# Optimization experiments

Hardware: AMD Instinct MI355X
Metric: run time of the kernel (lower is better)

The kernel has to match this reference:

```python
import jax, jax.numpy as jnp
import numpy as np

HIDDEN = 1024

def setup_inputs() -> dict:
    key = jax.random.key(0)
    k1, k2, k3 = jax.random.split(key, 3)
    X = jax.random.normal(k1, (4, 2048, HIDDEN), dtype=jnp.float32)
    W = jax.random.normal(k2, (HIDDEN, 3 * HIDDEN), dtype=jnp.float32) * (1.0 / np.sqrt(HIDDEN))
    b = jax.random.normal(k3, (3 * HIDDEN,), dtype=jnp.float32) * 0.02
    return {"X": X, "W": W, "b": b}

def reference(X, W, b):
    D = X.shape[-1]
    # fused QKV projection: [B,S,3D]
    QKV = jnp.einsum('bsd,de->bse', X, W) + b
    Q, K, V = jnp.split(QKV, 3, axis=-1)
    # full attention scores [B,S,S]
    scores = jnp.einsum('bqd,bkd->bqk', Q, K) / jnp.sqrt(jnp.float32(D))
    attn = jax.nn.softmax(scores, axis=-1)
    out = jnp.einsum('bqk,bkd->bqd', attn, V)
    return out
```

## Files before the change

### kernel.cpp

```cpp
#include <hip/hip_runtime.h>

typedef unsigned short u16;
typedef unsigned int   u32;
typedef __attribute__((ext_vector_type(8)))  short bf16x8;
typedef __attribute__((ext_vector_type(16))) float f32x16;
typedef __attribute__((ext_vector_type(4)))  unsigned short us4;

__device__ __forceinline__ u16 f2bf(float f) {
    union { float f; u32 u; } v; v.f = f;
    u32 u = v.u;
    return (u16)((u + 0x7fffu + ((u >> 16) & 1u)) >> 16);
}
__device__ __forceinline__ float bf2f_lo(u32 p) {
    union { u32 u; float f; } t; t.u = p << 16; return t.f;
}
__device__ __forceinline__ float bf2f_hi(u32 p) {
    union { u32 u; float f; } t; t.u = p & 0xffff0000u; return t.f;
}

__device__ __forceinline__ void gload_lds16(const void* g, void* l) {
    __builtin_amdgcn_global_load_lds((const __attribute__((address_space(1))) u32*)g,
                                     (__attribute__((address_space(3))) u32*)l,
                                     16, 0, 0);
}

template<int MINW, bool OUT_BF16, bool ADD_BIAS, bool PROJ, int MODE>
__global__ __launch_bounds__(256, MINW)
void gemm256(const u16* __restrict__ A, int lda, size_t strA,
             const u16* __restrict__ B, int ldb, size_t strB,
             void* __restrict__ Cv, int ldc, size_t strC,
             u16* __restrict__ Vtp,
             const float* __restrict__ bias, int K, float alpha)
{
    __shared__ __align__(16) u16 As[2][256 * 32];
    __shared__ __align__(16) u16 Bs[2][128 * 32];

    const int tid  = threadIdx.x;
    const int w    = tid >> 6;
    const int lane = tid & 63;
    const int wm   = w >> 1, wn = w & 1;
    const int l31  = lane & 31, lh = lane >> 5;

    const u32 id = blockIdx.x, x = id & 7, j = id >> 3;
    int mb, nb, bb;
    if (MODE == 0) { bb = 0;             mb = 8 * (int)(j & 3) + (int)x;        nb = (int)(j >> 2); }
    else           { bb = (int)(x >> 1); mb = 2 * (int)(j & 3) + (int)(x & 1);  nb = (int)(j >> 2); }
    const int m0 = mb * 256, n0 = nb * 128;

    A += (size_t)bb * strA;
    B += (size_t)bb * strB;

    size_t goffA[4], goffB[2];
#pragma unroll
    for (int h = 0; h < 4; ++h) {
        const int c = h * 256 + w * 64 + lane;
        const int r = c >> 2;
        const int q = ((c & 3) - (r >> 1)) & 3;
        goffA[h] = (size_t)(m0 + r) * lda + q * 8;
    }
#pragma unroll
    for (int h = 0; h < 2; ++h) {
        const int c = h * 256 + w * 64 + lane;
        const int r = c >> 2;
        const int q = ((c & 3) - (r >> 1)) & 3;
        goffB[h] = (size_t)(n0 + r) * ldb + q * 8;
    }

    int offA[4][2], offB[2][2];
#pragma unroll
    for (int i = 0; i < 4; ++i) {
        const int ra = wm * 128 + i * 32 + l31;
#pragma unroll
        for (int ks = 0; ks < 2; ++ks)
            offA[i][ks] = (ra * 4 + ((ks * 2 + lh + (ra >> 1)) & 3)) * 16;
    }
#pragma unroll
    for (int jj = 0; jj < 2; ++jj) {
        const int rb = wn * 64 + jj * 32 + l31;
#pragma unroll
        for (int ks = 0; ks < 2; ++ks)
            offB[jj][ks] = (rb * 4 + ((ks * 2 + lh + (rb >> 1)) & 3)) * 16;
    }

    f32x16 acc[4][2] = {};

#pragma unroll
    for (int h = 0; h < 4; ++h)
        gload_lds16(A + goffA[h], (char*)As[0] + (h * 256 + w * 64) * 16);
#pragma unroll
    for (int h = 0; h < 2; ++h)
        gload_lds16(B + goffB[h], (char*)Bs[0] + (h * 256 + w * 64) * 16);

    int cur = 0;
    for (int k0 = 0; k0 < K; k0 += 32) {
        __syncthreads();

        const int nk = k0 + 32;
        if (nk < K) {
#pragma unroll
            for (int h = 0; h < 4; ++h)
                gload_lds16(A + goffA[h] + nk, (char*)As[cur ^ 1] + (h * 256 + w * 64) * 16);
#pragma unroll
            for (int h = 0; h < 2; ++h)
                gload_lds16(B + goffB[h] + nk, (char*)Bs[cur ^ 1] + (h * 256 + w * 64) * 16);
        }

        const u16* Ac = As[cur]; const u16* Bc = Bs[cur];
#pragma unroll
        for (int ks = 0; ks < 2; ++ks) {
            bf16x8 af[4], bfr[2];
#pragma unroll
            for (int i = 0; i < 4; ++i)
                af[i] = *(const bf16x8*)((const char*)Ac + offA[i][ks]);
#pragma unroll
            for (int jj = 0; jj < 2; ++jj)
                bfr[jj] = *(const bf16x8*)((const char*)Bc + offB[jj][ks]);
#pragma unroll
            for (int i = 0; i < 4; ++i)
#pragma unroll
                for (int jj = 0; jj < 2; ++jj)
                    acc[i][jj] = __builtin_amdgcn_mfma_f32_32x32x16_bf16(
                        af[i], bfr[jj], acc[i][jj], 0, 0, 0);
        }
        cur ^= 1;
    }

    float bval[2];
    if (ADD_BIAS) {
#pragma unroll
        for (int jj = 0; jj < 2; ++jj) bval[jj] = bias[n0 + wn * 64 + jj * 32 + l31];
    }
    const bool vt = PROJ && (n0 >= 2048);
#pragma unroll
    for (int i = 0; i < 4; ++i) {
        const int rowb = m0 + wm * 128 + i * 32 + 4 * lh;
#pragma unroll
        for (int jj = 0; jj < 2; ++jj) {
            const int col = n0 + wn * 64 + jj * 32 + l31;
            if (vt) {
                const int b = rowb >> 11;
                u16* dst = Vtp + ((size_t)(b * 1024) + (col - 2048)) * 2048 + (rowb & 2047);
#pragma unroll
                for (int g = 0; g < 4; ++g) {
                    us4 o = { f2bf(acc[i][jj][4 * g + 0] + bval[jj]),
                              f2bf(acc[i][jj][4 * g + 1] + bval[jj]),
                              f2bf(acc[i][jj][4 * g + 2] + bval[jj]),
                              f2bf(acc[i][jj][4 * g + 3] + bval[jj]) };
                    *(us4*)(dst + 8 * g) = o;
                }
            } else {
#pragma unroll
                for (int r = 0; r < 16; ++r) {
                    const int row = rowb + (r & 3) + 8 * (r >> 2);
                    float v = acc[i][jj][r] * alpha;
                    if (ADD_BIAS) v += bval[jj];
                    if (OUT_BF16)
                        ((u16*)Cv)[(size_t)bb * strC + (size_t)row * ldc + col] = f2bf(v);
                    else
                        ((float*)Cv)[(size_t)bb * strC + (size_t)row * ldc + col] = v;
                }
            }
        }
    }
}

__global__ __launch_bounds__(512, 4)
void gemm128s(const u16* __restrict__ A, int lda, size_t strA,
              const u16* __restrict__ B, int ldb, size_t strB,
              float* __restrict__ C, int ldc, size_t strC)
{
    __shared__ __align__(16) char smem[65536];

    const int tid  = threadIdx.x;
    const int sub  = tid >> 8;
    const int t    = tid & 255;
    const int w    = t >> 6;
    const int lane = t & 63;
    const int wm   = w >> 1, wn = w & 1;
    const int l31  = lane & 31, lh = lane >> 5;

    const u32 id = blockIdx.x, x = id & 7, j = id >> 3;
    const int bb = (int)(x >> 1);
    const int mb = 2 * (int)(j & 7) + (int)(x & 1);
    const int nb = (int)(j >> 3);
    const int m0 = mb * 128, n0 = nb * 128;

    A += (size_t)bb * strA + sub * 1024;
    B += (size_t)bb * strB + sub * 1024;

    u16* As = (u16*)(smem + sub * 16384);
    u16* Bs = (u16*)(smem + sub * 16384 + 8192);

    size_t goffA[2], goffB[2];
#pragma unroll
    for (int h = 0; h < 2; ++h) {
        const int c = h * 256 + t;
        const int r = c >> 2;
        const int q = ((c & 3) - (r >> 1)) & 3;
        goffA[h] = (size_t)(m0 + r) * lda + q * 8;
        goffB[h] = (size_t)(n0 + r) * ldb + q * 8;
    }

    int offA[2][2], offB[2][2];
#pragma unroll
    for (int i = 0; i < 2; ++i) {
        const int ra = wm * 64 + i * 32 + l31;
        const int rb = wn * 64 + i * 32 + l31;
#pragma unroll
        for (int ks = 0; ks < 2; ++ks) {
            const int qq = ks * 2 + lh;
            offA[i][ks] = (ra * 4 + ((qq + (ra >> 1)) & 3)) * 16;
            offB[i][ks] = (rb * 4 + ((qq + (rb >> 1)) & 3)) * 16;
        }
    }

    f32x16 acc[2][2] = {};

    for (int k0 = 0; k0 < 1024; k0 += 32) {
#pragma unroll
        for (int h = 0; h < 2; ++h) {
            gload_lds16(A + goffA[h] + k0, (char*)As + (h * 256 + w * 64) * 16);
            gload_lds16(B + goffB[h] + k0, (char*)Bs + (h * 256 + w * 64) * 16);
        }
        __syncthreads();

#pragma unroll
        for (int ks = 0; ks < 2; ++ks) {
            bf16x8 af[2], bfr[2];
#pragma unroll
            for (int i = 0; i < 2; ++i) {
                af[i]  = *(const bf16x8*)((const char*)As + offA[i][ks]);
                bfr[i] = *(const bf16x8*)((const char*)Bs + offB[i][ks]);
            }
#pragma unroll
            for (int i = 0; i < 2; ++i)
#pragma unroll
                for (int jj = 0; jj < 2; ++jj)
                    acc[i][jj] = __builtin_amdgcn_mfma_f32_32x32x16_bf16(
                        af[i], bfr[jj], acc[i][jj], 0, 0, 0);
        }
        __syncthreads();
    }

    float* red = (float*)smem;
    if (sub == 1) {
#pragma unroll
        for (int c = 0; c < 16; ++c) {
            const int i = c >> 3, jj = (c >> 2) & 1, r0 = (c & 3) * 4;
            float4 v = { acc[i][jj][r0 + 0], acc[i][jj][r0 + 1],
                         acc[i][jj][r0 + 2], acc[i][jj][r0 + 3] };
            *(float4*)(red + t * 64 + ((c + t) & 15) * 4) = v;
        }
    }
    __syncthreads();
    if (sub == 0) {
#pragma unroll
        for (int c = 0; c < 16; ++c) {
            const int i = c >> 3, jj = (c >> 2) & 1, r0 = (c & 3) * 4;
            float4 v = *(const float4*)(red + t * 64 + ((c + t) & 15) * 4);
            acc[i][jj][r0 + 0] += v.x; acc[i][jj][r0 + 1] += v.y;
            acc[i][jj][r0 + 2] += v.z; acc[i][jj][r0 + 3] += v.w;
        }
#pragma unroll
        for (int i = 0; i < 2; ++i) {
            const int rowb = m0 + wm * 64 + i * 32 + 4 * lh;
#pragma unroll
            for (int jj = 0; jj < 2; ++jj) {
                const int col = n0 + wn * 64 + jj * 32 + l31;
#pragma unroll
                for (int r = 0; r < 16; ++r) {
                    const int row = rowb + (r & 3) + 8 * (r >> 2);
                    C[(size_t)bb * strC + (size_t)row * ldc + col] = acc[i][jj][r];
                }
            }
        }
    }
}

__global__ __launch_bounds__(256)
void convert_x(const float* __restrict__ X, u16* __restrict__ Xb, int n4)
{
    int i = blockIdx.x * blockDim.x + threadIdx.x;
    if (i < n4) {
        float4 v = ((const float4*)X)[i];
        us4 o = { f2bf(v.x), f2bf(v.y), f2bf(v.z), f2bf(v.w) };
        ((us4*)Xb)[i] = o;
    }
}

__global__ __launch_bounds__(256)
void transpose_w(const float* __restrict__ W, u16* __restrict__ Wt)
{
    __shared__ u16 t[64][65];
    const int k0 = blockIdx.x * 64, n0 = blockIdx.y * 64;
    const int tx = threadIdx.x, ty = threadIdx.y;
#pragma unroll
    for (int i = 0; i < 64; i += 4)
        t[ty + i][tx] = f2bf(W[(size_t)(k0 + ty + i) * 3072 + n0 + tx]);
    __syncthreads();
#pragma unroll
    for (int i = 0; i < 64; i += 4)
        Wt[(size_t)(n0 + ty + i) * 1024 + k0 + tx] = t[tx][ty + i];
}

__global__ __launch_bounds__(256)
void softmax_rows(u16* __restrict__ S)
{
    __shared__ float redm[4], reds[4];
    u16* sr = S + (size_t)blockIdx.x * 2048;
    const int t = threadIdx.x;

    uint4 raw = ((const uint4*)sr)[t];
    float xx[8];
    xx[0] = bf2f_lo(raw.x); xx[1] = bf2f_hi(raw.x);
    xx[2] = bf2f_lo(raw.y); xx[3] = bf2f_hi(raw.y);
    xx[4] = bf2f_lo(raw.z); xx[5] = bf2f_hi(raw.z);
    xx[6] = bf2f_lo(raw.w); xx[7] = bf2f_hi(raw.w);

    float mx = fmaxf(fmaxf(fmaxf(xx[0], xx[1]), fmaxf(xx[2], xx[3])),
                     fmaxf(fmaxf(xx[4], xx[5]), fmaxf(xx[6], xx[7])));
#pragma unroll
    for (int o = 32; o; o >>= 1) mx = fmaxf(mx, __shfl_xor(mx, o));
    if ((t & 63) == 0) redm[t >> 6] = mx;
    __syncthreads();
    mx = fmaxf(fmaxf(redm[0], redm[1]), fmaxf(redm[2], redm[3]));

    float e[8], s = 0.f;
#pragma unroll
    for (int k = 0; k < 8; ++k) { e[k] = __expf(xx[k] - mx); s += e[k]; }
#pragma unroll
    for (int o = 32; o; o >>= 1) s += __shfl_xor(s, o);
    if ((t & 63) == 0) reds[t >> 6] = s;
    __syncthreads();
    s = reds[0] + reds[1] + reds[2] + reds[3];
    const float inv = 1.0f / s;

    uint4 o4;
    o4.x = (u32)f2bf(e[0] * inv) | ((u32)f2bf(e[1] * inv) << 16);
    o4.y = (u32)f2bf(e[2] * inv) | ((u32)f2bf(e[3] * inv) << 16);
    o4.z = (u32)f2bf(e[4] * inv) | ((u32)f2bf(e[5] * inv) << 16);
    o4.w = (u32)f2bf(e[6] * inv) | ((u32)f2bf(e[7] * inv) << 16);
    ((uint4*)sr)[t] = o4;
}

extern "C" void kernel_launch(void* const* d_in, const int* in_sizes, int n_in,
                              void* d_out, int out_size, void* d_ws, size_t ws_size,
                              hipStream_t stream)
{
    const float* X    = (const float*)d_in[0];
    const float* W    = (const float*)d_in[1];
    const float* bias = (const float*)d_in[2];
    float* out = (float*)d_out;
    char* ws = (char*)d_ws;

    u16* QK = (u16*)ws;
    u16* Vt = (u16*)(ws + 33554432);
    u16* S  = (u16*)(ws + 50331648);
    u16* Xb = (u16*)(ws + 50331648);
    u16* Wt = (u16*)(ws + 67108864);

    convert_x<<<8192, 256, 0, stream>>>(X, Xb, 8192 * 1024 / 4);
    transpose_w<<<dim3(16, 48), dim3(64, 4), 0, stream>>>(W, Wt);

    gemm256<3, true, true, true, 0><<<768, 256, 0, stream>>>(
        Xb, 1024, 0, Wt, 1024, 0, QK, 2048, 0, Vt, bias, 1024, 1.0f);

    gemm256<2, true, false, false, 2><<<512, 256, 0, stream>>>(
        QK,        2048, (size_t)2048 * 2048,
        QK + 1024, 2048, (size_t)2048 * 2048,
        S,         2048, (size_t)2048 * 2048,
        nullptr, nullptr, 1024, 0.03125f);

    softmax_rows<<<8192, 256, 0, stream>>>(S);

    gemm128s<<<512, 512, 0, stream>>>(
        S,  2048, (size_t)2048 * 2048,
        Vt, 2048, (size_t)1024 * 2048,
        out, 1024, (size_t)2048 * 1024);
}
```

Baseline: 255.3 us.

## Run score GEMM on split-K 128x128 kernel and merge prep launches

The QK^T score GEMM moves from the 256x128-tile kernel to the 512-thread split-K 128x128 kernel. That kernel is generalized with a K parameter, an alpha scale and an optional bf16 output, and runs with 1024 blocks for more parallelism and occupancy. The X conversion and W transpose kernels are merged into one launch with a block-index branch, and the projection GEMM is specialized with fixed constants. The trade-off is an extra LDS reduction between the two K halves in the score GEMM and smaller tiles with less reuse.

```diff
diff --git a/kernel.cpp b/kernel.cpp
--- a/kernel.cpp
+++ b/kernel.cpp
@@ -24,16 +24,14 @@
                                      16, 0, 0);
 }
 
-template<int MINW, bool OUT_BF16, bool ADD_BIAS, bool PROJ, int MODE>
-__global__ __launch_bounds__(256, MINW)
-void gemm256(const u16* __restrict__ A, int lda, size_t strA,
-             const u16* __restrict__ B, int ldb, size_t strB,
-             void* __restrict__ Cv, int ldc, size_t strC,
-             u16* __restrict__ Vtp,
-             const float* __restrict__ bias, int K, float alpha)
+__global__ __launch_bounds__(256, 3)
+void gemm_proj(const u16* __restrict__ A, const u16* __restrict__ B,
+               u16* __restrict__ QK, u16* __restrict__ Vtp,
+               const float* __restrict__ bias)
 {
     __shared__ __align__(16) u16 As[2][256 * 32];
     __shared__ __align__(16) u16 Bs[2][128 * 32];
+    const int K = 1024, lda = 1024, ldb = 1024;
 
     const int tid  = threadIdx.x;
     const int w    = tid >> 6;
@@ -42,13 +40,9 @@
     const int l31  = lane & 31, lh = lane >> 5;
 
     const u32 id = blockIdx.x, x = id & 7, j = id >> 3;
-    int mb, nb, bb;
-    if (MODE == 0) { bb = 0;             mb = 8 * (int)(j & 3) + (int)x;        nb = (int)(j >> 2); }
-    else           { bb = (int)(x >> 1); mb = 2 * (int)(j & 3) + (int)(x & 1);  nb = (int)(j >> 2); }
+    const int mb = 8 * (int)(j & 3) + (int)x;
+    const int nb = (int)(j >> 2);
     const int m0 = mb * 256, n0 = nb * 128;
-
-    A += (size_t)bb * strA;
-    B += (size_t)bb * strB;
 
     size_t goffA[4], goffB[2];
 #pragma unroll
@@ -126,11 +120,9 @@
     }
 
     float bval[2];
-    if (ADD_BIAS) {
-#pragma unroll
-        for (int jj = 0; jj < 2; ++jj) bval[jj] = bias[n0 + wn * 64 + jj * 32 + l31];
-    }
-    const bool vt = PROJ && (n0 >= 2048);
+#pragma unroll
+    for (int jj = 0; jj < 2; ++jj) bval[jj] = bias[n0 + wn * 64 + jj * 32 + l31];
+    const bool vt = (n0 >= 2048);
 #pragma unroll
     for (int i = 0; i < 4; ++i) {
         const int rowb = m0 + wm * 128 + i * 32 + 4 * lh;
@@ -152,22 +144,19 @@
 #pragma unroll
                 for (int r = 0; r < 16; ++r) {
                     const int row = rowb + (r & 3) + 8 * (r >> 2);
-                    float v = acc[i][jj][r] * alpha;
-                    if (ADD_BIAS) v += bval[jj];
-                    if (OUT_BF16)
-                        ((u16*)Cv)[(size_t)bb * strC + (size_t)row * ldc + col] = f2bf(v);
-                    else
-                        ((float*)Cv)[(size_t)bb * strC + (size_t)row * ldc + col] = v;
+                    QK[(size_t)row * 2048 + col] = f2bf(acc[i][jj][r] + bval[jj]);
                 }
             }
         }
     }
 }
 
+template<bool OUT_BF16>
 __global__ __launch_bounds__(512, 4)
 void gemm128s(const u16* __restrict__ A, int lda, size_t strA,
               const u16* __restrict__ B, int ldb, size_t strB,
-              float* __restrict__ C, int ldc, size_t strC)
+              void* __restrict__ Cv, int ldc, size_t strC,
+              int K, float alpha)
 {
     __shared__ __align__(16) char smem[65536];
 
@@ -185,8 +174,9 @@
     const int nb = (int)(j >> 3);
     const int m0 = mb * 128, n0 = nb * 128;
 
-    A += (size_t)bb * strA + sub * 1024;
-    B += (size_t)bb * strB + sub * 1024;
+    const int Kh = K >> 1;
+    A += (size_t)bb * strA + sub * Kh;
+    B += (size_t)bb * strB + sub * Kh;
 
     u16* As = (u16*)(smem + sub * 16384);
     u16* Bs = (u16*)(smem + sub * 16384 + 8192);
@@ -216,7 +206,7 @@
 
     f32x16 acc[2][2] = {};
 
-    for (int k0 = 0; k0 < 1024; k0 += 32) {
+    for (int k0 = 0; k0 < Kh; k0 += 32) {
 #pragma unroll
         for (int h = 0; h < 2; ++h) {
             gload_lds16(A + goffA[h] + k0, (char*)As + (h * 256 + w * 64) * 16);
@@ -270,7 +260,11 @@
 #pragma unroll
                 for (int r = 0; r < 16; ++r) {
                     const int row = rowb + (r & 3) + 8 * (r >> 2);
-                    C[(size_t)bb * strC + (size_t)row * ldc + col] = acc[i][jj][r];
+                    const float v = acc[i][jj][r] * alpha;
+                    if (OUT_BF16)
+                        ((u16*)Cv)[(size_t)bb * strC + (size_t)row * ldc + col] = f2bf(v);
+                    else
+                        ((float*)Cv)[(size_t)bb * strC + (size_t)row * ldc + col] = v;
                 }
             }
         }
@@ -278,29 +272,28 @@
 }
 
 __global__ __launch_bounds__(256)
-void convert_x(const float* __restrict__ X, u16* __restrict__ Xb, int n4)
-{
-    int i = blockIdx.x * blockDim.x + threadIdx.x;
-    if (i < n4) {
+void prep(const float* __restrict__ X, u16* __restrict__ Xb,
+          const float* __restrict__ W, u16* __restrict__ Wt)
+{
+    const int bid = blockIdx.x;
+    if (bid < 8192) {
+        const int i = bid * 256 + threadIdx.x;
         float4 v = ((const float4*)X)[i];
         us4 o = { f2bf(v.x), f2bf(v.y), f2bf(v.z), f2bf(v.w) };
         ((us4*)Xb)[i] = o;
-    }
-}
-
-__global__ __launch_bounds__(256)
-void transpose_w(const float* __restrict__ W, u16* __restrict__ Wt)
-{
-    __shared__ u16 t[64][65];
-    const int k0 = blockIdx.x * 64, n0 = blockIdx.y * 64;
-    const int tx = threadIdx.x, ty = threadIdx.y;
-#pragma unroll
-    for (int i = 0; i < 64; i += 4)
-        t[ty + i][tx] = f2bf(W[(size_t)(k0 + ty + i) * 3072 + n0 + tx]);
-    __syncthreads();
-#pragma unroll
-    for (int i = 0; i < 64; i += 4)
-        Wt[(size_t)(n0 + ty + i) * 1024 + k0 + tx] = t[tx][ty + i];
+    } else {
+        __shared__ u16 t[64][65];
+        const int b  = bid - 8192;
+        const int k0 = (b & 15) * 64, n0 = (b >> 4) * 64;
+        const int tx = threadIdx.x & 63, ty = threadIdx.x >> 6;
+#pragma unroll
+        for (int i = 0; i < 64; i += 4)
+            t[ty + i][tx] = f2bf(W[(size_t)(k0 + ty + i) * 3072 + n0 + tx]);
+        __syncthreads();
+#pragma unroll
+        for (int i = 0; i < 64; i += 4)
+            Wt[(size_t)(n0 + ty + i) * 1024 + k0 + tx] = t[tx][ty + i];
+    }
 }
 
 __global__ __launch_bounds__(256)
@@ -359,22 +352,21 @@
     u16* Xb = (u16*)(ws + 50331648);
     u16* Wt = (u16*)(ws + 67108864);
 
-    convert_x<<<8192, 256, 0, stream>>>(X, Xb, 8192 * 1024 / 4);
-    transpose_w<<<dim3(16, 48), dim3(64, 4), 0, stream>>>(W, Wt);
-
-    gemm256<3, true, true, true, 0><<<768, 256, 0, stream>>>(
-        Xb, 1024, 0, Wt, 1024, 0, QK, 2048, 0, Vt, bias, 1024, 1.0f);
-
-    gemm256<2, true, false, false, 2><<<512, 256, 0, stream>>>(
+    prep<<<8960, 256, 0, stream>>>(X, Xb, W, Wt);
+
+    gemm_proj<<<768, 256, 0, stream>>>(Xb, Wt, QK, Vt, bias);
+
+    gemm128s<true><<<1024, 512, 0, stream>>>(
         QK,        2048, (size_t)2048 * 2048,
         QK + 1024, 2048, (size_t)2048 * 2048,
         S,         2048, (size_t)2048 * 2048,
-        nullptr, nullptr, 1024, 0.03125f);
+        1024, 0.03125f);
 
     softmax_rows<<<8192, 256, 0, stream>>>(S);
 
-    gemm128s<<<512, 512, 0, stream>>>(
+    gemm128s<false><<<512, 512, 0, stream>>>(
         S,  2048, (size_t)2048 * 2048,
         Vt, 2048, (size_t)1024 * 2048,
-        out, 1024, (size_t)2048 * 1024);
-}
+        out, 1024, (size_t)2048 * 1024,
+        2048, 1.0f);
+}
```

New measurement: 269.5 us. 5.6% more time.

## Fuse softmax into QK epilogue and PV GEMM with deferred normalization

Applied to the files above, without the earlier changes.

Drops the separate softmax kernel. The QK^T GEMM epilogue now writes exp(scores) directly, without subtracting the row max. The PV GEMM sums the bf16 exponentials per row from its A-tile fragments, reduces them through LDS atomics, and divides the output by the row sums in its epilogue. This removes a full read and write of the score matrix plus one launch, at the cost of extra VALU work in the PV inner loop. Skipping the max subtraction risks overflow when scores are large.

```diff
diff --git a/kernel.cpp b/kernel.cpp
--- a/kernel.cpp
+++ b/kernel.cpp
@@ -17,6 +17,14 @@
 __device__ __forceinline__ float bf2f_hi(u32 p) {
     union { u32 u; float f; } t; t.u = p & 0xffff0000u; return t.f;
 }
+__device__ __forceinline__ float sum8bf(bf16x8 v) {
+    union { bf16x8 b; u32 d[4]; } u; u.b = v;
+    float s0 = bf2f_lo(u.d[0]) + bf2f_hi(u.d[0]);
+    float s1 = bf2f_lo(u.d[1]) + bf2f_hi(u.d[1]);
+    float s2 = bf2f_lo(u.d[2]) + bf2f_hi(u.d[2]);
+    float s3 = bf2f_lo(u.d[3]) + bf2f_hi(u.d[3]);
+    return (s0 + s1) + (s2 + s3);
+}
 
 __device__ __forceinline__ void gload_lds16(const void* g, void* l) {
     __builtin_amdgcn_global_load_lds((const __attribute__((address_space(1))) u32*)g,
@@ -24,7 +32,7 @@
                                      16, 0, 0);
 }
 
-template<int MINW, bool OUT_BF16, bool ADD_BIAS, bool PROJ, int MODE>
+template<int MINW, bool OUT_BF16, bool ADD_BIAS, bool PROJ, int MODE, bool EXPO>
 __global__ __launch_bounds__(256, MINW)
 void gemm256(const u16* __restrict__ A, int lda, size_t strA,
              const u16* __restrict__ B, int ldb, size_t strB,
@@ -154,6 +162,7 @@
                     const int row = rowb + (r & 3) + 8 * (r >> 2);
                     float v = acc[i][jj][r] * alpha;
                     if (ADD_BIAS) v += bval[jj];
+                    if (EXPO)     v = __expf(v);
                     if (OUT_BF16)
                         ((u16*)Cv)[(size_t)bb * strC + (size_t)row * ldc + col] = f2bf(v);
                     else
@@ -165,9 +174,9 @@
 }
 
 __global__ __launch_bounds__(512, 4)
-void gemm128s(const u16* __restrict__ A, int lda, size_t strA,
-              const u16* __restrict__ B, int ldb, size_t strB,
-              float* __restrict__ C, int ldc, size_t strC)
+void gemm_pv(const u16* __restrict__ A, int lda, size_t strA,
+             const u16* __restrict__ B, int ldb, size_t strB,
+             float* __restrict__ C, int ldc, size_t strC, int K)
 {
     __shared__ __align__(16) char smem[65536];
 
@@ -185,8 +194,9 @@
     const int nb = (int)(j >> 3);
     const int m0 = mb * 128, n0 = nb * 128;
 
-    A += (size_t)bb * strA + sub * 1024;
-    B += (size_t)bb * strB + sub * 1024;
+    const int Kh = K >> 1;
+    A += (size_t)bb * strA + sub * Kh;
+    B += (size_t)bb * strB + sub * Kh;
 
     u16* As = (u16*)(smem + sub * 16384);
     u16* Bs = (u16*)(smem + sub * 16384 + 8192);
@@ -215,8 +225,9 @@
     }
 
     f32x16 acc[2][2] = {};
-
-    for (int k0 = 0; k0 < 1024; k0 += 32) {
+    float rs0 = 0.f, rs1 = 0.f;
+
+    for (int k0 = 0; k0 < Kh; k0 += 32) {
 #pragma unroll
         for (int h = 0; h < 2; ++h) {
             gload_lds16(A + goffA[h] + k0, (char*)As + (h * 256 + w * 64) * 16);
@@ -232,6 +243,7 @@
                 af[i]  = *(const bf16x8*)((const char*)As + offA[i][ks]);
                 bfr[i] = *(const bf16x8*)((const char*)Bs + offB[i][ks]);
             }
+            if (wn == 0) { rs0 += sum8bf(af[0]); rs1 += sum8bf(af[1]); }
 #pragma unroll
             for (int i = 0; i < 2; ++i)
 #pragma unroll
@@ -261,16 +273,37 @@
             acc[i][jj][r0 + 0] += v.x; acc[i][jj][r0 + 1] += v.y;
             acc[i][jj][r0 + 2] += v.z; acc[i][jj][r0 + 3] += v.w;
         }
+    }
+    __syncthreads();
+
+    float* rsL = (float*)smem;
+    if (tid < 128) rsL[tid] = 0.f;
+    __syncthreads();
+    if (wn == 0) {
+        rs0 += __shfl_xor(rs0, 32);
+        rs1 += __shfl_xor(rs1, 32);
+        if (lh == 0) {
+            atomicAdd(&rsL[wm * 64 + l31],      rs0);
+            atomicAdd(&rsL[wm * 64 + 32 + l31], rs1);
+        }
+    }
+    __syncthreads();
+
+    if (sub == 0) {
 #pragma unroll
         for (int i = 0; i < 2; ++i) {
-            const int rowb = m0 + wm * 64 + i * 32 + 4 * lh;
+            const int rb = wm * 64 + i * 32 + 4 * lh;
+            float inv[16];
+#pragma unroll
+            for (int r = 0; r < 16; ++r)
+                inv[r] = 1.0f / rsL[rb + (r & 3) + 8 * (r >> 2)];
 #pragma unroll
             for (int jj = 0; jj < 2; ++jj) {
                 const int col = n0 + wn * 64 + jj * 32 + l31;
 #pragma unroll
                 for (int r = 0; r < 16; ++r) {
-                    const int row = rowb + (r & 3) + 8 * (r >> 2);
-                    C[(size_t)bb * strC + (size_t)row * ldc + col] = acc[i][jj][r];
+                    const int row = m0 + rb + (r & 3) + 8 * (r >> 2);
+                    C[(size_t)bb * strC + (size_t)row * ldc + col] = acc[i][jj][r] * inv[r];
                 }
             }
         }
@@ -303,46 +336,6 @@
         Wt[(size_t)(n0 + ty + i) * 1024 + k0 + tx] = t[tx][ty + i];
 }
 
-__global__ __launch_bounds__(256)
-void softmax_rows(u16* __restrict__ S)
-{
-    __shared__ float redm[4], reds[4];
-    u16* sr = S + (size_t)blockIdx.x * 2048;
-    const int t = threadIdx.x;
-
-    uint4 raw = ((const uint4*)sr)[t];
-    float xx[8];
-    xx[0] = bf2f_lo(raw.x); xx[1] = bf2f_hi(raw.x);
-    xx[2] = bf2f_lo(raw.y); xx[3] = bf2f_hi(raw.y);
-    xx[4] = bf2f_lo(raw.z); xx[5] = bf2f_hi(raw.z);
-    xx[6] = bf2f_lo(raw.w); xx[7] = bf2f_hi(raw.w);
-
-    float mx = fmaxf(fmaxf(fmaxf(xx[0], xx[1]), fmaxf(xx[2], xx[3])),
-                     fmaxf(fmaxf(xx[4], xx[5]), fmaxf(xx[6], xx[7])));
-#pragma unroll
-    for (int o = 32; o; o >>= 1) mx = fmaxf(mx, __shfl_xor(mx, o));
-    if ((t & 63) == 0) redm[t >> 6] = mx;
-    __syncthreads();
-    mx = fmaxf(fmaxf(redm[0], redm[1]), fmaxf(redm[2], redm[3]));
-
-    float e[8], s = 0.f;
-#pragma unroll
-    for (int k = 0; k < 8; ++k) { e[k] = __expf(xx[k] - mx); s += e[k]; }
-#pragma unroll
-    for (int o = 32; o; o >>= 1) s += __shfl_xor(s, o);
-    if ((t & 63) == 0) reds[t >> 6] = s;
-    __syncthreads();
-    s = reds[0] + reds[1] + reds[2] + reds[3];
-    const float inv = 1.0f / s;
-
-    uint4 o4;
-    o4.x = (u32)f2bf(e[0] * inv) | ((u32)f2bf(e[1] * inv) << 16);
-    o4.y = (u32)f2bf(e[2] * inv) | ((u32)f2bf(e[3] * inv) << 16);
-    o4.z = (u32)f2bf(e[4] * inv) | ((u32)f2bf(e[5] * inv) << 16);
-    o4.w = (u32)f2bf(e[6] * inv) | ((u32)f2bf(e[7] * inv) << 16);
-    ((uint4*)sr)[t] = o4;
-}
-
 extern "C" void kernel_launch(void* const* d_in, const int* in_sizes, int n_in,
                               void* d_out, int out_size, void* d_ws, size_t ws_size,
                               hipStream_t stream)
@@ -355,26 +348,25 @@
 
     u16* QK = (u16*)ws;
     u16* Vt = (u16*)(ws + 33554432);
-    u16* S  = (u16*)(ws + 50331648);
+    u16* E  = (u16*)(ws + 50331648);
     u16* Xb = (u16*)(ws + 50331648);
     u16* Wt = (u16*)(ws + 67108864);
 
     convert_x<<<8192, 256, 0, stream>>>(X, Xb, 8192 * 1024 / 4);
     transpose_w<<<dim3(16, 48), dim3(64, 4), 0, stream>>>(W, Wt);
 
-    gemm256<3, true, true, true, 0><<<768, 256, 0, stream>>>(
+    gemm256<3, true, true, true, 0, false><<<768, 256, 0, stream>>>(
         Xb, 1024, 0, Wt, 1024, 0, QK, 2048, 0, Vt, bias, 1024, 1.0f);
 
-    gemm256<2, true, false, false, 2><<<512, 256, 0, stream>>>(
+    gemm256<2, true, false, false, 2, true><<<512, 256, 0, stream>>>(
         QK,        2048, (size_t)2048 * 2048,
         QK + 1024, 2048, (size_t)2048 * 2048,
-        S,         2048, (size_t)2048 * 2048,
+        E,         2048, (size_t)2048 * 2048,
         nullptr, nullptr, 1024, 0.03125f);
 
-    softmax_rows<<<8192, 256, 0, stream>>>(S);
-
-    gemm128s<<<512, 512, 0, stream>>>(
-        S,  2048, (size_t)2048 * 2048,
+    gemm_pv<<<512, 512, 0, stream>>>(
+        E,  2048, (size_t)2048 * 2048,
         Vt, 2048, (size_t)1024 * 2048,
-        out, 1024, (size_t)2048 * 1024);
-}
+        out, 1024, (size_t)2048 * 1024,
+        2048);
+}
```

After: 248.7 us. -2.6%, faster.
